# Performance work log

Hardware: AMD Instinct MI355X
Metric: run time of the kernel (lower is better)

Reference implementation:

```python
import jax, jax.numpy as jnp
import numpy as np

V = 32000; D = 256; H = 8; L = 2; FF = 1024; S = 512; B = 32
M = 4096          # mem_max_entries
NC = 10           # num_classes
K = 4             # retrieve top-k
TH = 0.5          # write threshold
EPS = 1e-8


def setup_inputs() -> dict:
    key = jax.random.key(0)
    ks = jax.random.split(key, 24)
    s = 0.02
    def nrm(k, shape):
        return jax.random.normal(k, shape, jnp.float32) * s
    return {
        "input_ids": jax.random.randint(ks[0], (B, S), 0, V),
        "tok_emb": nrm(ks[1], (V, D)),
        "pos_emb": nrm(ks[2], (S, D)),
        # per-layer params stacked on leading dim L
        "Wqkv": nrm(ks[3], (L, 3 * D, D)), "bqkv": jnp.zeros((L, 3 * D)),
        "Wo": nrm(ks[4], (L, D, D)), "bo": jnp.zeros((L, D)),
        "ln1_g": jnp.ones((L, D)), "ln1_b": jnp.zeros((L, D)),
        "W1": nrm(ks[5], (L, FF, D)), "b1": jnp.zeros((L, FF)),
        "W2": nrm(ks[6], (L, D, FF)), "b2": jnp.zeros((L, D)),
        "ln2_g": jnp.ones((L, D)), "ln2_b": jnp.zeros((L, D)),
        # write gate MLP (d -> d -> 1, sigmoid)
        "Wg1": nrm(ks[7], (D, D)), "bg1": jnp.zeros((D,)),
        "Wg2": nrm(ks[8], (1, D)), "bg2": jnp.zeros((1,)),
        # classifier
        "Wc": nrm(ks[9], (NC, D)), "bc": jnp.zeros((NC,)),
    }


def _layer_norm(x, g, b):
    m = x.mean(-1, keepdims=True)
    v = ((x - m) ** 2).mean(-1, keepdims=True)
    return (x - m) / jnp.sqrt(v + 1e-5) * g + b


def _encoder_layer(x, Wqkv, bqkv, Wo, bo, g1, b1, W1, bf1, W2, bf2, g2, b2):
    # post-LN TransformerEncoderLayer, relu activation, batch_first
    Bx, Sx, Dx = x.shape
    dh = Dx // H
    qkv = x @ Wqkv.T + bqkv                     # [B,S,3D]
    q, k, v = jnp.split(qkv, 3, axis=-1)
    def heads(t):
        return t.reshape(Bx, Sx, H, dh).transpose(0, 2, 1, 3)  # [B,H,S,dh]
    q, k, v = heads(q), heads(k), heads(v)
    scores = jnp.einsum("bhqd,bhkd->bhqk", q, k) / jnp.sqrt(jnp.float32(dh))
    attn = jax.nn.softmax(scores, axis=-1)
    o = jnp.einsum("bhqk,bhkd->bhqd", attn, v)
    o = o.transpose(0, 2, 1, 3).reshape(Bx, Sx, Dx)
    o = o @ Wo.T + bo
    x = _layer_norm(x + o, g1, b1)
    ff = jax.nn.relu(x @ W1.T + bf1) @ W2.T + bf2
    return _layer_norm(x + ff, g2, b2)


def reference(input_ids, tok_emb, pos_emb, Wqkv, bqkv, Wo, bo, ln1_g, ln1_b,
              W1, b1, W2, b2, ln2_g, ln2_b, Wg1, bg1, Wg2, bg2, Wc, bc):
    Bx, Sx = input_ids.shape
    x = tok_emb[input_ids] + pos_emb[jnp.arange(Sx)][None, :, :]
    for l in range(L):
        x = _encoder_layer(x, Wqkv[l], bqkv[l], Wo[l], bo[l], ln1_g[l], ln1_b[l],
                           W1[l], b1[l], W2[l], b2[l], ln2_g[l], ln2_b[l])
    h = x                                        # [B,S,D]
    cls_state = h[:, 0, :]                       # [B,D]

    # --- write gate: per-token store into external memory (capped FIFO scatter) ---
    flat_h = h.reshape(-1, D)                    # [B*S, D]
    probs = jax.nn.sigmoid(jax.nn.relu(flat_h @ Wg1.T + bg1) @ Wg2.T + bg2)[:, 0]
    mask = probs > TH                            # [B*S]
    slot = jnp.cumsum(mask.astype(jnp.int32)) - 1
    valid = mask & (slot < M)
    idx = jnp.where(valid, slot, M)              # overflow -> dummy row M
    mem = jnp.zeros((M + 1, D), jnp.float32).at[idx].set(flat_h)[:M]
    count = jnp.minimum(mask.sum(), M)
    occupied = jnp.arange(M) < count             # [M]

    # --- top-k cosine retrieval with CLS as query ---
    qn = cls_state / (jnp.linalg.norm(cls_state, axis=-1, keepdims=True) + EPS)
    kn = mem / (jnp.linalg.norm(mem, axis=-1, keepdims=True) + EPS)
    sims = qn @ kn.T                             # [B,M]
    sims = jnp.where(occupied[None, :], sims, -1e9)
    top_sims, top_idx = jax.lax.top_k(sims, K)   # [B,K]
    vals = mem[top_idx]                          # [B,K,D] (unoccupied rows are zero)
    attn = jax.nn.softmax(top_sims, axis=-1)
    mem_vec = jnp.einsum("bk,bkd->bd", attn, vals)
    mem_vec = jnp.where(count > 0, mem_vec, 0.0)

    cls_aug = cls_state + mem_vec
    return cls_aug @ Wc.T + bc                   # [B,NC]
```

## Files before the change

kernel.cpp:

```cpp
#include <hip/hip_runtime.h>
#include <math.h>

#define D_   256
#define H_   8
#define L_   2
#define FF_  1024
#define S_   512
#define B_   32
#define M_   4096
#define NC_  10
#define ROWS (B_*S_)

typedef __attribute__((ext_vector_type(8))) short bf16x8;
typedef __attribute__((ext_vector_type(4))) float f32x4;
typedef unsigned int uint32;

__device__ __forceinline__ float wave_sum(float v) {
#pragma unroll
  for (int off = 1; off < 64; off <<= 1) v += __shfl_xor(v, off, 64);
  return v;
}

__device__ __forceinline__ unsigned short bf16_rne(float x) {
  unsigned int b = __float_as_uint(x);
  return (unsigned short)((b + 0x7FFFu + ((b >> 16) & 1u)) >> 16);
}
__device__ __forceinline__ float bf16_f(unsigned short h) {
  return __uint_as_float(((unsigned int)h) << 16);
}
__device__ __forceinline__ uint32 pack_split(float x) {
  const unsigned short h = bf16_rne(x);
  const unsigned short l = bf16_rne(x - bf16_f(h));
  return (uint32)h | ((uint32)l << 16);
}
__device__ __forceinline__ float unsplit(uint32 p) {
  return __uint_as_float(p << 16) + __uint_as_float(p & 0xffff0000u);
}
__device__ __forceinline__ void unpack_store(unsigned short* Hq, unsigned short* Lq,
                                             int off, uint4 v) {
  uint2 hp, lp;
  hp.x = (v.x & 0xffffu) | (v.y << 16);
  hp.y = (v.z & 0xffffu) | (v.w << 16);
  lp.x = (v.x >> 16) | (v.y & 0xffff0000u);
  lp.y = (v.z >> 16) | (v.w & 0xffff0000u);
  *(uint2*)&Hq[off] = hp;
  *(uint2*)&Lq[off] = lp;
}
__device__ __forceinline__ bf16x8 ld_frag(const unsigned short* p, int off) {
  union { uint2 u[2]; bf16x8 v; } x;
  x.u[0] = *(const uint2*)(p + off);
  x.u[1] = *(const uint2*)(p + off + 4);
  return x.v;
}

__global__ __launch_bounds__(256) void pack_f32(const float* __restrict__ src,
                                                uint32* __restrict__ dst, int n4) {
  const int i = blockIdx.x * 256 + threadIdx.x;
  if (i < n4) {
    const float4 v = ((const float4*)src)[i];
    uint4 o;
    o.x = pack_split(v.x); o.y = pack_split(v.y);
    o.z = pack_split(v.z); o.w = pack_split(v.w);
    ((uint4*)dst)[i] = o;
  }
}

__global__ __launch_bounds__(256) void emb_kernel(const int* __restrict__ ids,
                                                  const float* __restrict__ tok,
                                                  const float* __restrict__ pos,
                                                  uint32* __restrict__ xp) {
  const int row  = blockIdx.x * 4 + (threadIdx.x >> 6);
  const int lane = threadIdx.x & 63;
  const int id = ids[row];
  const int s  = row & (S_ - 1);
  const float4 t = *(const float4*)(tok + (size_t)id * D_ + lane * 4);
  const float4 p = *(const float4*)(pos + (size_t)s  * D_ + lane * 4);
  uint4 o;
  o.x = pack_split(t.x + p.x); o.y = pack_split(t.y + p.y);
  o.z = pack_split(t.z + p.z); o.w = pack_split(t.w + p.w);
  *(uint4*)(xp + (size_t)row * D_ + lane * 4) = o;
}

#define LP 36
template<int RELU>
__global__ __launch_bounds__(256, 2) void gemm_mfma(const uint32* __restrict__ Ap,
                                                    const uint32* __restrict__ Bp,
                                                    const float* __restrict__ bias,
                                                    uint32* __restrict__ Cp,
                                                    int K, int N, int NX) {
  __shared__ __align__(16) unsigned short Ah[128 * LP];
  __shared__ __align__(16) unsigned short Al[128 * LP];
  __shared__ __align__(16) unsigned short Bh[128 * LP];
  __shared__ __align__(16) unsigned short Bl[128 * LP];

  const int q8 = gridDim.x >> 3;
  const int orig = (blockIdx.x & 7) * q8 + (blockIdx.x >> 3);
  const int by = orig / NX, bx = orig % NX;
  const int m0 = by * 128, n0 = bx * 128;

  const int tid  = threadIdx.x;
  const int lane = tid & 63;
  const int wid  = tid >> 6;
  const int wm = wid >> 1, wn = wid & 1;
  const int lrow  = lane & 15;
  const int khalf = (lane >> 4) * 8;

  const int srow = tid >> 3;
  const int kq   = (tid & 7) << 2;
  const uint32* Aptr = Ap + (size_t)(m0 + srow) * K + kq;
  const uint32* Bptr = Bp + (size_t)(n0 + srow) * K + kq;

  f32x4 acc[4][4];
#pragma unroll
  for (int i = 0; i < 4; i++)
#pragma unroll
    for (int j = 0; j < 4; j++) acc[i][j] = (f32x4){0.f, 0.f, 0.f, 0.f};

  uint4 pa[4], pb[4];
#pragma unroll
  for (int j = 0; j < 4; j++) {
    pa[j] = *(const uint4*)(Aptr + (size_t)j * 32 * K);
    pb[j] = *(const uint4*)(Bptr + (size_t)j * 32 * K);
  }

  for (int k0 = 0; k0 < K; k0 += 32) {
    const int kn = (k0 + 32 < K) ? (k0 + 32) : k0;
    uint4 na[4], nb[4];
#pragma unroll
    for (int j = 0; j < 4; j++) {
      na[j] = *(const uint4*)(Aptr + (size_t)j * 32 * K + kn);
      nb[j] = *(const uint4*)(Bptr + (size_t)j * 32 * K + kn);
    }

    __syncthreads();
#pragma unroll
    for (int j = 0; j < 4; j++) {
      unpack_store(Ah, Al, (srow + j * 32) * LP + kq, pa[j]);
      unpack_store(Bh, Bl, (srow + j * 32) * LP + kq, pb[j]);
    }
    __syncthreads();

    bf16x8 ah[4], al[4], bh[4], bl[4];
#pragma unroll
    for (int f = 0; f < 4; f++) {
      const int rA = (wm * 64 + f * 16 + lrow) * LP + khalf;
      const int rB = (wn * 64 + f * 16 + lrow) * LP + khalf;
      ah[f] = ld_frag(Ah, rA);
      al[f] = ld_frag(Al, rA);
      bh[f] = ld_frag(Bh, rB);
      bl[f] = ld_frag(Bl, rB);
    }
#pragma unroll
    for (int fm = 0; fm < 4; fm++)
#pragma unroll
      for (int fn = 0; fn < 4; fn++) {
        acc[fm][fn] = __builtin_amdgcn_mfma_f32_16x16x32_bf16(ah[fm], bh[fn], acc[fm][fn], 0, 0, 0);
        acc[fm][fn] = __builtin_amdgcn_mfma_f32_16x16x32_bf16(ah[fm], bl[fn], acc[fm][fn], 0, 0, 0);
        acc[fm][fn] = __builtin_amdgcn_mfma_f32_16x16x32_bf16(al[fm], bh[fn], acc[fm][fn], 0, 0, 0);
      }
#pragma unroll
    for (int j = 0; j < 4; j++) { pa[j] = na[j]; pb[j] = nb[j]; }
  }

#pragma unroll
  for (int fm = 0; fm < 4; fm++)
#pragma unroll
    for (int fn = 0; fn < 4; fn++) {
      const int mrow = m0 + wm * 64 + fm * 16 + (lane >> 4) * 4;
      const int ncol = n0 + wn * 64 + fn * 16 + (lane & 15);
      const float bi = bias[ncol];
#pragma unroll
      for (int r = 0; r < 4; r++) {
        float v = acc[fm][fn][r] + bi;
        if (RELU) v = fmaxf(v, 0.f);
        Cp[(size_t)(mrow + r) * N + ncol] = pack_split(v);
      }
    }
}

template<int MODE>
__global__ __launch_bounds__(512, 2) void gemm_ln(const uint32* __restrict__ Ap,
                                                  const uint32* __restrict__ Bp,
                                                  const float* __restrict__ bias,
                                                  const uint32* __restrict__ residP,
                                                  const float* __restrict__ g,
                                                  const float* __restrict__ beta,
                                                  const float* __restrict__ Wg2,
                                                  const float* __restrict__ bg2,
                                                  uint32* __restrict__ outP,
                                                  int* __restrict__ mask,
                                                  int K) {
  __shared__ __align__(16) unsigned short Ah[64 * LP];
  __shared__ __align__(16) unsigned short Al[64 * LP];
  __shared__ __align__(16) unsigned short Bh[256 * LP];
  __shared__ __align__(16) unsigned short Bl[256 * LP];
  __shared__ float psumS[4][64];
  __shared__ float psumQ[4][64];
  __shared__ float meanL[64];
  __shared__ float invL[64];

  const int q8 = gridDim.x >> 3;
  const int m0 = ((blockIdx.x & 7) * q8 + (blockIdx.x >> 3)) * 64;

  const int tid  = threadIdx.x;
  const int lane = tid & 63;
  const int wid  = tid >> 6;
  const int wm = wid >> 2, wn = wid & 3;
  const int lrow  = lane & 15;
  const int khalf = (lane >> 4) * 8;

  const int srow = tid >> 3;
  const int kq   = (tid & 7) << 2;
  const uint32* Aptr = Ap + (size_t)(m0 + srow) * K + kq;
  const uint32* Bptr = Bp + (size_t)srow * K + kq;

  f32x4 acc[2][4];
#pragma unroll
  for (int i = 0; i < 2; i++)
#pragma unroll
    for (int j = 0; j < 4; j++) acc[i][j] = (f32x4){0.f, 0.f, 0.f, 0.f};

  uint4 pa, pb[4];
  pa = *(const uint4*)Aptr;
#pragma unroll
  for (int j = 0; j < 4; j++) pb[j] = *(const uint4*)(Bptr + (size_t)j * 64 * K);

  for (int k0 = 0; k0 < K; k0 += 32) {
    const int kn = (k0 + 32 < K) ? (k0 + 32) : k0;
    uint4 na, nb[4];
    na = *(const uint4*)(Aptr + kn);
#pragma unroll
    for (int j = 0; j < 4; j++) nb[j] = *(const uint4*)(Bptr + (size_t)j * 64 * K + kn);

    __syncthreads();
    unpack_store(Ah, Al, srow * LP + kq, pa);
#pragma unroll
    for (int j = 0; j < 4; j++)
      unpack_store(Bh, Bl, (srow + j * 64) * LP + kq, pb[j]);
    __syncthreads();

    bf16x8 ah[2], al[2], bh[4], bl[4];
#pragma unroll
    for (int fm = 0; fm < 2; fm++) {
      const int r = (wm * 32 + fm * 16 + lrow) * LP + khalf;
      ah[fm] = ld_frag(Ah, r);
      al[fm] = ld_frag(Al, r);
    }
#pragma unroll
    for (int fn = 0; fn < 4; fn++) {
      const int r = (wn * 64 + fn * 16 + lrow) * LP + khalf;
      bh[fn] = ld_frag(Bh, r);
      bl[fn] = ld_frag(Bl, r);
    }
#pragma unroll
    for (int fm = 0; fm < 2; fm++)
#pragma unroll
      for (int fn = 0; fn < 4; fn++) {
        acc[fm][fn] = __builtin_amdgcn_mfma_f32_16x16x32_bf16(ah[fm], bh[fn], acc[fm][fn], 0, 0, 0);
        acc[fm][fn] = __builtin_amdgcn_mfma_f32_16x16x32_bf16(ah[fm], bl[fn], acc[fm][fn], 0, 0, 0);
        acc[fm][fn] = __builtin_amdgcn_mfma_f32_16x16x32_bf16(al[fm], bh[fn], acc[fm][fn], 0, 0, 0);
      }
    pa = na;
#pragma unroll
    for (int j = 0; j < 4; j++) pb[j] = nb[j];
  }

  int cc[4];
  float bi[4];
#pragma unroll
  for (int fn = 0; fn < 4; fn++) {
    cc[fn] = wn * 64 + fn * 16 + (lane & 15);
    bi[fn] = bias[cc[fn]];
  }

  float vv[2][4][4];
  float rs[2][4], rq[2][4];

  if (MODE == 0) {
#pragma unroll
    for (int fm = 0; fm < 2; fm++)
#pragma unroll
      for (int r = 0; r < 4; r++) {
        const int row = m0 + wm * 32 + fm * 16 + (lane >> 4) * 4 + r;
        float s = 0.f, q = 0.f;
#pragma unroll
        for (int fn = 0; fn < 4; fn++) {
          const float rx = unsplit(residP[(size_t)row * 256 + cc[fn]]);
          const float a = acc[fm][fn][r] + bi[fn] + rx;
          vv[fm][fn][r] = a;
          s += a; q += a * a;
        }
        rs[fm][r] = s; rq[fm][r] = q;
      }
  } else {
    float wg[4];
#pragma unroll
    for (int fn = 0; fn < 4; fn++) wg[fn] = Wg2[cc[fn]];
#pragma unroll
    for (int fm = 0; fm < 2; fm++)
#pragma unroll
      for (int r = 0; r < 4; r++) {
        float s = 0.f;
#pragma unroll
        for (int fn = 0; fn < 4; fn++)
          s += fmaxf(acc[fm][fn][r] + bi[fn], 0.f) * wg[fn];
        rs[fm][r] = s;
      }
  }

#pragma unroll
  for (int off = 1; off < 16; off <<= 1) {
#pragma unroll
    for (int fm = 0; fm < 2; fm++)
#pragma unroll
      for (int r = 0; r < 4; r++) {
        rs[fm][r] += __shfl_xor(rs[fm][r], off, 64);
        if (MODE == 0) rq[fm][r] += __shfl_xor(rq[fm][r], off, 64);
      }
  }
  if ((lane & 15) == 0) {
#pragma unroll
    for (int fm = 0; fm < 2; fm++)
#pragma unroll
      for (int r = 0; r < 4; r++) {
        const int rloc = wm * 32 + fm * 16 + (lane >> 4) * 4 + r;
        psumS[wn][rloc] = rs[fm][r];
        if (MODE == 0) psumQ[wn][rloc] = rq[fm][r];
      }
  }
  __syncthreads();
  if (tid < 64) {
    float s = 0.f, q = 0.f;
#pragma unroll
    for (int w = 0; w < 4; w++) {
      s += psumS[w][tid];
      if (MODE == 0) q += psumQ[w][tid];
    }
    if (MODE == 0) {
      const float mean = s * (1.f / 256.f);
      const float var = q * (1.f / 256.f) - mean * mean;
      meanL[tid] = mean;
      invL[tid] = rsqrtf(var + 1e-5f);
    } else {
      mask[m0 + tid] = (s + bg2[0]) > 0.f ? 1 : 0;
    }
  }
  if (MODE == 0) {
    __syncthreads();
#pragma unroll
    for (int fm = 0; fm < 2; fm++)
#pragma unroll
      for (int r = 0; r < 4; r++) {
        const int rloc = wm * 32 + fm * 16 + (lane >> 4) * 4 + r;
        const int row = m0 + rloc;
        const float mu = meanL[rloc], iv = invL[rloc];
#pragma unroll
        for (int fn = 0; fn < 4; fn++) {
          const float y = (vv[fm][fn][r] - mu) * iv * g[cc[fn]] + beta[cc[fn]];
          outP[(size_t)row * 256 + cc[fn]] = pack_split(y);
        }
      }
  }
}

#define KP 36
#define VP 516
__global__ __launch_bounds__(1024, 4) void attn_mfma(const uint32* __restrict__ qkv,
                                                     uint32* __restrict__ o) {
  __shared__ __align__(16) unsigned short Kh[512 * KP];
  __shared__ __align__(16) unsigned short Kl[512 * KP];
  __shared__ __align__(16) unsigned short Vth[32 * VP];
  __shared__ __align__(16) unsigned short Vtl[32 * VP];

  const int q8g = gridDim.x >> 3;
  const int obh = (blockIdx.x & 7) * q8g + (blockIdx.x >> 3);
  const int b = obh >> 3, h = obh & 7;
  const int tid = threadIdx.x;
  const int lane = tid & 63;
  const int wv = tid >> 6;
  const uint32* base = qkv + (size_t)b * (S_ * 768) + h * 32;

  if (tid < 512) {
    const int slot = tid;
    const int s5 = slot & 31;
    const int orig = (slot & ~31) + 8 * ((s5 >> 2) & 3) + ((s5 >> 4) << 2) + (s5 & 3);
    const uint32* p = base + (size_t)orig * 768 + 256;
#pragma unroll
    for (int j = 0; j < 8; j++)
      unpack_store(Kh, Kl, slot * KP + j * 4, *(const uint4*)(p + j * 4));
  } else {
    const int u  = tid - 512;
    const int kp = u & 255;
    const int dg = (u >> 8) * 16;
    const uint32* p0 = base + (size_t)(2 * kp) * 768 + 512 + dg;
    const uint32* p1 = p0 + 768;
    union { uint4 u4[4]; uint32 w[16]; } a0, a1;
#pragma unroll
    for (int i = 0; i < 4; i++) {
      a0.u4[i] = *(const uint4*)(p0 + i * 4);
      a1.u4[i] = *(const uint4*)(p1 + i * 4);
    }
#pragma unroll
    for (int d = 0; d < 16; d++) {
      const uint32 w0 = a0.w[d], w1 = a1.w[d];
      *(uint32*)&Vth[(dg + d) * VP + 2 * kp] = (w0 & 0xffffu) | (w1 << 16);
      *(uint32*)&Vtl[(dg + d) * VP + 2 * kp] = (w0 >> 16) | (w1 & 0xffff0000u);
    }
  }

  const int q0 = wv * 32;
  bf16x8 qh[2], ql[2];
#pragma unroll
  for (int f = 0; f < 2; f++) {
    const uint32* qp = base + (size_t)(q0 + f * 16 + (lane & 15)) * 768 + ((lane >> 4) * 8);
    union { uint4 u4[2]; uint32 w[8]; } qu;
    qu.u4[0] = *(const uint4*)qp;
    qu.u4[1] = *(const uint4*)(qp + 4);
    bf16x8 vh, vl;
#pragma unroll
    for (int j = 0; j < 8; j++) {
      const float qf = unsplit(qu.w[j]);
      const float sv = qf * 0.17677669529663687f;
      const unsigned short hh = bf16_rne(sv);
      vh[j] = (short)hh;
      vl[j] = (short)bf16_rne(sv - bf16_f(hh));
    }
    qh[f] = vh; ql[f] = vl;
  }

  __syncthreads();

  f32x4 oacc[2][2];
#pragma unroll
  for (int i = 0; i < 2; i++)
#pragma unroll
    for (int j = 0; j < 2; j++) oacc[i][j] = (f32x4){0.f, 0.f, 0.f, 0.f};
  float lacc[2] = {0.f, 0.f};

  for (int kt = 0; kt < S_; kt += 32) {
    bf16x8 kah[2], kal[2];
#pragma unroll
    for (int u = 0; u < 2; u++) {
      const int off = (kt + u * 16 + (lane & 15)) * KP + ((lane >> 4) * 8);
      kah[u] = ld_frag(Kh, off);
      kal[u] = ld_frag(Kl, off);
    }
    bf16x8 vah[2], val[2];
#pragma unroll
    for (int df = 0; df < 2; df++) {
      const int off = (df * 16 + (lane & 15)) * VP + kt + ((lane >> 4) * 8);
      vah[df] = ld_frag(Vth, off);
      val[df] = ld_frag(Vtl, off);
    }
    f32x4 s[2][2];
#pragma unroll
    for (int u = 0; u < 2; u++)
#pragma unroll
      for (int f = 0; f < 2; f++) {
        f32x4 a = (f32x4){0.f, 0.f, 0.f, 0.f};
        a = __builtin_amdgcn_mfma_f32_16x16x32_bf16(kal[u], qh[f], a, 0, 0, 0);
        a = __builtin_amdgcn_mfma_f32_16x16x32_bf16(kah[u], ql[f], a, 0, 0, 0);
        a = __builtin_amdgcn_mfma_f32_16x16x32_bf16(kah[u], qh[f], a, 0, 0, 0);
        s[u][f] = a;
      }
#pragma unroll
    for (int f = 0; f < 2; f++) {
      union { uint32 w[4]; bf16x8 v; } ph, pl;
#pragma unroll
      for (int u = 0; u < 2; u++) {
        const float p0 = __expf(s[u][f][0]);
        const float p1 = __expf(s[u][f][1]);
        const float p2 = __expf(s[u][f][2]);
        const float p3 = __expf(s[u][f][3]);
        lacc[f] += (p0 + p1) + (p2 + p3);
        unsigned int h01, h23;
        asm volatile("v_cvt_pk_bf16_f32 %0, %1, %2" : "=v"(h01) : "v"(p0), "v"(p1));
        asm volatile("v_cvt_pk_bf16_f32 %0, %1, %2" : "=v"(h23) : "v"(p2), "v"(p3));
        const float r0 = p0 - __uint_as_float(h01 << 16);
        const float r1 = p1 - __uint_as_float(h01 & 0xffff0000u);
        const float r2 = p2 - __uint_as_float(h23 << 16);
        const float r3 = p3 - __uint_as_float(h23 & 0xffff0000u);
        unsigned int l01, l23;
        asm volatile("v_cvt_pk_bf16_f32 %0, %1, %2" : "=v"(l01) : "v"(r0), "v"(r1));
        asm volatile("v_cvt_pk_bf16_f32 %0, %1, %2" : "=v"(l23) : "v"(r2), "v"(r3));
        ph.w[u * 2 + 0] = h01;
        ph.w[u * 2 + 1] = h23;
        pl.w[u * 2 + 0] = l01;
        pl.w[u * 2 + 1] = l23;
      }
#pragma unroll
      for (int df = 0; df < 2; df++) {
        oacc[df][f] = __builtin_amdgcn_mfma_f32_16x16x32_bf16(val[df], ph.v, oacc[df][f], 0, 0, 0);
        oacc[df][f] = __builtin_amdgcn_mfma_f32_16x16x32_bf16(vah[df], pl.v, oacc[df][f], 0, 0, 0);
        oacc[df][f] = __builtin_amdgcn_mfma_f32_16x16x32_bf16(vah[df], ph.v, oacc[df][f], 0, 0, 0);
      }
    }
  }

#pragma unroll
  for (int f = 0; f < 2; f++) {
    lacc[f] += __shfl_xor(lacc[f], 16, 64);
    lacc[f] += __shfl_xor(lacc[f], 32, 64);
  }
#pragma unroll
  for (int f = 0; f < 2; f++) {
    const float inv = 1.f / lacc[f];
    const int q = q0 + f * 16 + (lane & 15);
    uint32* op = o + (size_t)(b * S_ + q) * D_ + h * 32;
#pragma unroll
    for (int df = 0; df < 2; df++) {
      const int dbase = df * 16 + (lane >> 4) * 4;
#pragma unroll
      for (int r = 0; r < 4; r++)
        op[dbase + r] = pack_split(oacc[df][f][r] * inv);
    }
  }
}

__global__ __launch_bounds__(256) void scan_kernel(const int* __restrict__ mask,
                                                   int* __restrict__ slots,
                                                   int* __restrict__ countp) {
  __shared__ int wtot[4];
  const int tid = threadIdx.x;
  const int lane = tid & 63, wid = tid >> 6;
  const int base = tid * 64;
  int s = 0;
#pragma unroll 8
  for (int i = 0; i < 64; i++) s += mask[base + i];
  int inc = s;
#pragma unroll
  for (int off = 1; off < 64; off <<= 1) {
    const int t = __shfl_up(inc, off, 64);
    if (lane >= off) inc += t;
  }
  if (lane == 63) wtot[wid] = inc;
  __syncthreads();
  int woff = 0;
#pragma unroll
  for (int w = 0; w < 4; w++) woff += (w < wid) ? wtot[w] : 0;
  const int total = wtot[0] + wtot[1] + wtot[2] + wtot[3];
  if (tid == 0) countp[0] = total < M_ ? total : M_;
  int run = woff + inc - s;
  for (int i = 0; i < 64; i++) {
    const int r = base + i;
    const int mk = mask[r];
    slots[r] = (mk && run < M_) ? run : -1;
    run += mk;
  }
}

__global__ __launch_bounds__(256) void scatter_kernel(const uint32* __restrict__ h,
                                                      const int* __restrict__ slots,
                                                      float* __restrict__ mem) {
  const int row  = blockIdx.x * 4 + (threadIdx.x >> 6);
  const int lane = threadIdx.x & 63;
  const int sl = slots[row];
  if (sl >= 0) {
    const uint4 p = *(const uint4*)(h + (size_t)row * D_ + lane * 4);
    float4 r;
    r.x = unsplit(p.x); r.y = unsplit(p.y);
    r.z = unsplit(p.z); r.w = unsplit(p.w);
    *(float4*)(mem + (size_t)sl * D_ + lane * 4) = r;
  }
}

__global__ __launch_bounds__(256) void qnorm_kernel(const uint32* __restrict__ h,
                                                    float* __restrict__ qden) {
  const int b    = blockIdx.x * 4 + (threadIdx.x >> 6);
  const int lane = threadIdx.x & 63;
  const uint4 p = *(const uint4*)(h + (size_t)b * S_ * D_ + lane * 4);
  const float x0 = unsplit(p.x), x1 = unsplit(p.y);
  const float x2 = unsplit(p.z), x3 = unsplit(p.w);
  float sq = x0 * x0 + x1 * x1 + x2 * x2 + x3 * x3;
  sq = wave_sum(sq);
  if (lane == 0) qden[b] = sqrtf(sq) + 1e-8f;
}

__global__ __launch_bounds__(256) void sims_kernel(const uint32* __restrict__ h,
                                                   const float* __restrict__ mem,
                                                   const float* __restrict__ qden,
                                                   const int* __restrict__ countp,
                                                   float* __restrict__ sims) {
  __shared__ float cls[B_ * D_];
  __shared__ float qd[B_];
  const int tid = threadIdx.x;
  const int lane = tid & 63, wid = tid >> 6;
  for (int i = tid; i < B_ * D_ / 4; i += 256) {
    const int flat = i * 4;
    const int b = flat >> 8, d = flat & 255;
    const uint4 p = *(const uint4*)(h + (size_t)b * S_ * D_ + d);
    float4 r;
    r.x = unsplit(p.x); r.y = unsplit(p.y);
    r.z = unsplit(p.z); r.w = unsplit(p.w);
    *(float4*)&cls[flat] = r;
  }
  if (tid < B_) qd[tid] = qden[tid];
  __syncthreads();
  const int count = countp[0];
  const int r = blockIdx.x * 4 + wid;
  const float4 m4 = *(const float4*)(mem + (size_t)r * D_ + lane * 4);
  float sq = m4.x * m4.x + m4.y * m4.y + m4.z * m4.z + m4.w * m4.w;
  sq = wave_sum(sq);
  const float rn = sqrtf(sq) + 1e-8f;
  if (r < count) {
    for (int b = 0; b < B_; b++) {
      const float4 c4 = *(const float4*)&cls[b * D_ + lane * 4];
      float dt = m4.x * c4.x + m4.y * c4.y + m4.z * c4.z + m4.w * c4.w;
      dt = wave_sum(dt);
      if (lane == 0) sims[b * M_ + r] = dt / (qd[b] * rn);
    }
  } else if (lane == 0) {
    for (int b = 0; b < B_; b++) sims[b * M_ + r] = -1e9f;
  }
}

__global__ __launch_bounds__(256) void topk_mix(const uint32* __restrict__ h,
                                                const float* __restrict__ mem,
                                                const float* __restrict__ simsg,
                                                const int* __restrict__ countp,
                                                const float* __restrict__ Wc,
                                                const float* __restrict__ bc,
                                                float* __restrict__ out) {
  __shared__ float sims[M_];
  __shared__ float cls[D_];
  __shared__ float wv4[4];
  __shared__ int   wi4[4];
  __shared__ float aug[D_];
  __shared__ float tv[4];
  __shared__ int   tix[4];

  const int b = blockIdx.x, tid = threadIdx.x;
  const int lane = tid & 63, wid = tid >> 6;
  const int count = countp[0];

  for (int i = tid; i < M_; i += 256) sims[i] = simsg[b * M_ + i];
  cls[tid] = unsplit(h[(size_t)b * S_ * D_ + tid]);
  __syncthreads();

  for (int k = 0; k < 4; k++) {
    float bv = -INFINITY; int bi = 1 << 30;
#pragma unroll
    for (int rr = 0; rr < M_ / 256; rr++) {
      const int r = tid + rr * 256;
      const float v = sims[r];
      if (v > bv || (v == bv && r < bi)) { bv = v; bi = r; }
    }
#pragma unroll
    for (int off = 1; off < 64; off <<= 1) {
      const float ov = __shfl_xor(bv, off, 64);
      const int   oi = __shfl_xor(bi, off, 64);
      if (ov > bv || (ov == bv && oi < bi)) { bv = ov; bi = oi; }
    }
    if (lane == 0) { wv4[wid] = bv; wi4[wid] = bi; }
    __syncthreads();
    if (tid == 0) {
      float bb = wv4[0]; int bbi = wi4[0];
#pragma unroll
      for (int i = 1; i < 4; i++)
        if (wv4[i] > bb || (wv4[i] == bb && wi4[i] < bbi)) { bb = wv4[i]; bbi = wi4[i]; }
      tv[k] = bb; tix[k] = bbi; sims[bbi] = -INFINITY;
    }
    __syncthreads();
  }

  float w[4];
  {
    const float mx = tv[0];
    float ws = 0.f;
#pragma unroll
    for (int k = 0; k < 4; k++) { w[k] = expf(tv[k] - mx); ws += w[k]; }
    const float inv = 1.f / ws;
#pragma unroll
    for (int k = 0; k < 4; k++) w[k] *= inv;
  }

  {
    float mv = 0.f;
    if (count > 0) {
#pragma unroll
      for (int k = 0; k < 4; k++) mv = fmaf(w[k], mem[(size_t)tix[k] * D_ + tid], mv);
    }
    aug[tid] = cls[tid] + mv;
  }
  __syncthreads();

  const float4 a4 = *(const float4*)&aug[lane * 4];
  for (int c = wid; c < NC_; c += 4) {
    const float4 wc = *(const float4*)(Wc + (size_t)c * D_ + lane * 4);
    float dt = a4.x * wc.x + a4.y * wc.y + a4.z * wc.z + a4.w * wc.w;
    dt = wave_sum(dt);
    if (lane == 0) out[b * NC_ + c] = dt + bc[c];
  }
}

extern "C" void kernel_launch(void* const* d_in, const int* in_sizes, int n_in,
                              void* d_out, int out_size, void* d_ws, size_t ws_size,
                              hipStream_t stream) {
  const int*   ids  = (const int*)d_in[0];
  const float* tok  = (const float*)d_in[1];
  const float* pos  = (const float*)d_in[2];
  const float* Wqkv = (const float*)d_in[3];
  const float* bqkv = (const float*)d_in[4];
  const float* Wo   = (const float*)d_in[5];
  const float* bo   = (const float*)d_in[6];
  const float* ln1g = (const float*)d_in[7];
  const float* ln1b = (const float*)d_in[8];
  const float* W1   = (const float*)d_in[9];
  const float* b1   = (const float*)d_in[10];
  const float* W2   = (const float*)d_in[11];
  const float* b2   = (const float*)d_in[12];
  const float* ln2g = (const float*)d_in[13];
  const float* ln2b = (const float*)d_in[14];
  const float* Wg1  = (const float*)d_in[15];
  const float* bg1  = (const float*)d_in[16];
  const float* Wg2  = (const float*)d_in[17];
  const float* bg2  = (const float*)d_in[18];
  const float* Wc   = (const float*)d_in[19];
  const float* bc   = (const float*)d_in[20];
  float* out = (float*)d_out;

  uint32* xAp   = (uint32*)d_ws;
  uint32* xBp   = xAp + (size_t)ROWS * D_;
  uint32* obp   = xBp + (size_t)ROWS * D_;
  uint32* bigp  = obp + (size_t)ROWS * D_;
  uint32* Wqkvp = bigp + (size_t)ROWS * FF_;
  uint32* Wop   = Wqkvp + (size_t)L_ * 768 * 256;
  uint32* W1p   = Wop   + (size_t)L_ * 256 * 256;
  uint32* W2p   = W1p   + (size_t)L_ * 1024 * 256;
  uint32* Wg1p  = W2p   + (size_t)L_ * 256 * 1024;
  float*  mem   = (float*)(Wg1p + 256 * 256);
  float*  qden  = mem + (size_t)M_ * D_;
  float*  sims  = qden + 64;
  int*    mask  = (int*)(sims + (size_t)B_ * M_);
  int*    slots = mask + ROWS;
  int*    cnt   = slots + ROWS;

  pack_f32<<<(L_ * 768 * 256 / 4 + 255) / 256, 256, 0, stream>>>(Wqkv, Wqkvp, L_ * 768 * 256 / 4);
  pack_f32<<<(L_ * 256 * 256 / 4 + 255) / 256, 256, 0, stream>>>(Wo, Wop, L_ * 256 * 256 / 4);
  pack_f32<<<(L_ * 1024 * 256 / 4 + 255) / 256, 256, 0, stream>>>(W1, W1p, L_ * 1024 * 256 / 4);
  pack_f32<<<(L_ * 256 * 1024 / 4 + 255) / 256, 256, 0, stream>>>(W2, W2p, L_ * 256 * 1024 / 4);
  pack_f32<<<(256 * 256 / 4 + 255) / 256, 256, 0, stream>>>(Wg1, Wg1p, 256 * 256 / 4);

  emb_kernel<<<ROWS / 4, 256, 0, stream>>>(ids, tok, pos, xAp);

  for (int l = 0; l < L_; l++) {
    gemm_mfma<0><<<768, 256, 0, stream>>>(
        xAp, Wqkvp + (size_t)l * 768 * 256, bqkv + l * 768, bigp, 256, 768, 6);
    attn_mfma<<<B_ * H_, 1024, 0, stream>>>(bigp, obp);
    gemm_ln<0><<<ROWS / 64, 512, 0, stream>>>(
        obp, Wop + (size_t)l * 256 * 256, bo + l * 256, xAp,
        ln1g + l * 256, ln1b + l * 256, nullptr, nullptr, xBp, nullptr, 256);
    gemm_mfma<1><<<1024, 256, 0, stream>>>(
        xBp, W1p + (size_t)l * 1024 * 256, b1 + l * 1024, bigp, 256, 1024, 8);
    gemm_ln<0><<<ROWS / 64, 512, 0, stream>>>(
        bigp, W2p + (size_t)l * 256 * 1024, b2 + l * 256, xBp,
        ln2g + l * 256, ln2b + l * 256, nullptr, nullptr, xAp, nullptr, 1024);
  }

  gemm_ln<1><<<ROWS / 64, 512, 0, stream>>>(
      xAp, Wg1p, bg1, nullptr, nullptr, nullptr, Wg2, bg2, nullptr, mask, 256);
  scan_kernel<<<1, 256, 0, stream>>>(mask, slots, cnt);
  (void)hipMemsetAsync(mem, 0, (size_t)M_ * D_ * sizeof(float), stream);
  scatter_kernel<<<ROWS / 4, 256, 0, stream>>>(xAp, slots, mem);

  qnorm_kernel<<<B_ / 4, 256, 0, stream>>>(xAp, qden);
  sims_kernel<<<M_ / 4, 256, 0, stream>>>(xAp, mem, qden, cnt, sims);
  topk_mix<<<B_, 256, 0, stream>>>(xAp, mem, sims, cnt, Wc, bc, out);
}
```

Before: 408.4 us.

## Load A fragments directly from global memory into registers, bypassing LDS

Both GEMM kernels now have each wave read its A-operand MFMA fragments straight from global memory into registers and split them into hi/lo bf16 there. The A tiles no longer go through shared memory, which cuts LDS footprint and LDS store/load traffic. In exchange, A rows are fetched redundantly by the waves that share them (the two wn waves in gemm_mfma, the four wn waves in gemm_ln), and the loads are no longer software-prefetched a k-step ahead. Global latency is therefore exposed inside the loop, and the per-lane strided 16-byte reads coalesce less well.

```diff
diff --git a/kernel.cpp b/kernel.cpp
--- a/kernel.cpp
+++ b/kernel.cpp
@@ -45,6 +45,19 @@
   lp.y = (v.z >> 16) | (v.w & 0xffff0000u);
   *(uint2*)&Hq[off] = hp;
   *(uint2*)&Lq[off] = lp;
+}
+__device__ __forceinline__ void unpack_frag(const uint4 u0, const uint4 u1,
+                                            bf16x8* hi, bf16x8* lo) {
+  union { uint32 w[4]; bf16x8 v; } H, L;
+  H.w[0] = (u0.x & 0xffffu) | (u0.y << 16);
+  H.w[1] = (u0.z & 0xffffu) | (u0.w << 16);
+  H.w[2] = (u1.x & 0xffffu) | (u1.y << 16);
+  H.w[3] = (u1.z & 0xffffu) | (u1.w << 16);
+  L.w[0] = (u0.x >> 16) | (u0.y & 0xffff0000u);
+  L.w[1] = (u0.z >> 16) | (u0.w & 0xffff0000u);
+  L.w[2] = (u1.x >> 16) | (u1.y & 0xffff0000u);
+  L.w[3] = (u1.z >> 16) | (u1.w & 0xffff0000u);
+  *hi = H.v; *lo = L.v;
 }
 __device__ __forceinline__ bf16x8 ld_frag(const unsigned short* p, int off) {
   union { uint2 u[2]; bf16x8 v; } x;
@@ -88,8 +101,6 @@
                                                     const float* __restrict__ bias,
                                                     uint32* __restrict__ Cp,
                                                     int K, int N, int NX) {
-  __shared__ __align__(16) unsigned short Ah[128 * LP];
-  __shared__ __align__(16) unsigned short Al[128 * LP];
   __shared__ __align__(16) unsigned short Bh[128 * LP];
   __shared__ __align__(16) unsigned short Bl[128 * LP];
 
@@ -107,8 +118,8 @@
 
   const int srow = tid >> 3;
   const int kq   = (tid & 7) << 2;
-  const uint32* Aptr = Ap + (size_t)(m0 + srow) * K + kq;
   const uint32* Bptr = Bp + (size_t)(n0 + srow) * K + kq;
+  const uint32* Afrag = Ap + (size_t)(m0 + wm * 64 + lrow) * K + khalf;
 
   f32x4 acc[4][4];
 #pragma unroll
@@ -116,37 +127,35 @@
 #pragma unroll
     for (int j = 0; j < 4; j++) acc[i][j] = (f32x4){0.f, 0.f, 0.f, 0.f};
 
-  uint4 pa[4], pb[4];
-#pragma unroll
-  for (int j = 0; j < 4; j++) {
-    pa[j] = *(const uint4*)(Aptr + (size_t)j * 32 * K);
-    pb[j] = *(const uint4*)(Bptr + (size_t)j * 32 * K);
-  }
+  uint4 pb[4];
+#pragma unroll
+  for (int j = 0; j < 4; j++) pb[j] = *(const uint4*)(Bptr + (size_t)j * 32 * K);
 
   for (int k0 = 0; k0 < K; k0 += 32) {
+    uint4 ar[4][2];
+#pragma unroll
+    for (int f = 0; f < 4; f++) {
+      const uint32* p = Afrag + (size_t)(f * 16) * K + k0;
+      ar[f][0] = *(const uint4*)p;
+      ar[f][1] = *(const uint4*)(p + 4);
+    }
     const int kn = (k0 + 32 < K) ? (k0 + 32) : k0;
-    uint4 na[4], nb[4];
-#pragma unroll
-    for (int j = 0; j < 4; j++) {
-      na[j] = *(const uint4*)(Aptr + (size_t)j * 32 * K + kn);
+    uint4 nb[4];
+#pragma unroll
+    for (int j = 0; j < 4; j++)
       nb[j] = *(const uint4*)(Bptr + (size_t)j * 32 * K + kn);
-    }
 
     __syncthreads();
 #pragma unroll
-    for (int j = 0; j < 4; j++) {
-      unpack_store(Ah, Al, (srow + j * 32) * LP + kq, pa[j]);
+    for (int j = 0; j < 4; j++)
       unpack_store(Bh, Bl, (srow + j * 32) * LP + kq, pb[j]);
-    }
     __syncthreads();
 
     bf16x8 ah[4], al[4], bh[4], bl[4];
 #pragma unroll
     for (int f = 0; f < 4; f++) {
-      const int rA = (wm * 64 + f * 16 + lrow) * LP + khalf;
+      unpack_frag(ar[f][0], ar[f][1], &ah[f], &al[f]);
       const int rB = (wn * 64 + f * 16 + lrow) * LP + khalf;
-      ah[f] = ld_frag(Ah, rA);
-      al[f] = ld_frag(Al, rA);
       bh[f] = ld_frag(Bh, rB);
       bl[f] = ld_frag(Bl, rB);
     }
@@ -159,7 +168,7 @@
         acc[fm][fn] = __builtin_amdgcn_mfma_f32_16x16x32_bf16(al[fm], bh[fn], acc[fm][fn], 0, 0, 0);
       }
 #pragma unroll
-    for (int j = 0; j < 4; j++) { pa[j] = na[j]; pb[j] = nb[j]; }
+    for (int j = 0; j < 4; j++) pb[j] = nb[j];
   }
 
 #pragma unroll
@@ -190,8 +199,6 @@
                                                   uint32* __restrict__ outP,
                                                   int* __restrict__ mask,
                                                   int K) {
-  __shared__ __align__(16) unsigned short Ah[64 * LP];
-  __shared__ __align__(16) unsigned short Al[64 * LP];
   __shared__ __align__(16) unsigned short Bh[256 * LP];
   __shared__ __align__(16) unsigned short Bl[256 * LP];
   __shared__ float psumS[4][64];
@@ -211,8 +218,8 @@
 
   const int srow = tid >> 3;
   const int kq   = (tid & 7) << 2;
-  const uint32* Aptr = Ap + (size_t)(m0 + srow) * K + kq;
   const uint32* Bptr = Bp + (size_t)srow * K + kq;
+  const uint32* Afrag = Ap + (size_t)(m0 + wm * 32 + lrow) * K + khalf;
 
   f32x4 acc[2][4];
 #pragma unroll
@@ -220,20 +227,25 @@
 #pragma unroll
     for (int j = 0; j < 4; j++) acc[i][j] = (f32x4){0.f, 0.f, 0.f, 0.f};
 
-  uint4 pa, pb[4];
-  pa = *(const uint4*)Aptr;
+  uint4 pb[4];
 #pragma unroll
   for (int j = 0; j < 4; j++) pb[j] = *(const uint4*)(Bptr + (size_t)j * 64 * K);
 
   for (int k0 = 0; k0 < K; k0 += 32) {
+    uint4 ar[2][2];
+#pragma unroll
+    for (int f = 0; f < 2; f++) {
+      const uint32* p = Afrag + (size_t)(f * 16) * K + k0;
+      ar[f][0] = *(const uint4*)p;
+      ar[f][1] = *(const uint4*)(p + 4);
+    }
     const int kn = (k0 + 32 < K) ? (k0 + 32) : k0;
-    uint4 na, nb[4];
-    na = *(const uint4*)(Aptr + kn);
-#pragma unroll
-    for (int j = 0; j < 4; j++) nb[j] = *(const uint4*)(Bptr + (size_t)j * 64 * K + kn);
+    uint4 nb[4];
+#pragma unroll
+    for (int j = 0; j < 4; j++)
+      nb[j] = *(const uint4*)(Bptr + (size_t)j * 64 * K + kn);
 
     __syncthreads();
-    unpack_store(Ah, Al, srow * LP + kq, pa);
 #pragma unroll
     for (int j = 0; j < 4; j++)
       unpack_store(Bh, Bl, (srow + j * 64) * LP + kq, pb[j]);
@@ -241,11 +253,8 @@
 
     bf16x8 ah[2], al[2], bh[4], bl[4];
 #pragma unroll
-    for (int fm = 0; fm < 2; fm++) {
-      const int r = (wm * 32 + fm * 16 + lrow) * LP + khalf;
-      ah[fm] = ld_frag(Ah, r);
-      al[fm] = ld_frag(Al, r);
-    }
+    for (int fm = 0; fm < 2; fm++)
+      unpack_frag(ar[fm][0], ar[fm][1], &ah[fm], &al[fm]);
 #pragma unroll
     for (int fn = 0; fn < 4; fn++) {
       const int r = (wn * 64 + fn * 16 + lrow) * LP + khalf;
@@ -260,7 +269,6 @@
         acc[fm][fn] = __builtin_amdgcn_mfma_f32_16x16x32_bf16(ah[fm], bl[fn], acc[fm][fn], 0, 0, 0);
         acc[fm][fn] = __builtin_amdgcn_mfma_f32_16x16x32_bf16(al[fm], bh[fn], acc[fm][fn], 0, 0, 0);
       }
-    pa = na;
 #pragma unroll
     for (int j = 0; j < 4; j++) pb[j] = nb[j];
   }
```

After: 496.0 us. 21.5% more time.
